# Kernel tuning notes

Hardware: AMD Instinct MI355X
Metric: run time of the kernel (lower is better)

The kernel has to match this reference:

```python
import jax, jax.numpy as jnp
import numpy as np

B, S, H, DH = 2, 2048, 16, 64
D = H * DH


def setup_inputs() -> dict:
    key = jax.random.key(0)
    ks = jax.random.split(key, 10)
    std = 0.02
    return {
        "hidden_states": jax.random.normal(ks[0], (B, S, D), jnp.float32),
        "mask": jax.random.randint(ks[1], (B, S), 0, 2, jnp.int64 if jax.config.jax_enable_x64 else jnp.int32),
        "Wq": jax.random.normal(ks[2], (D, D), jnp.float32) * std,
        "bq": jnp.zeros((D,), jnp.float32),
        "Wk": jax.random.normal(ks[3], (D, D), jnp.float32) * std,
        "bk": jnp.zeros((D,), jnp.float32),
        "Wv": jax.random.normal(ks[4], (D, D), jnp.float32) * std,
        "bv": jnp.zeros((D,), jnp.float32),
        "Wo": jax.random.normal(ks[5], (D, D), jnp.float32) * std,
        "bo": jnp.zeros((D,), jnp.float32),
    }


def _split_heads(x):
    # (B, S, H*DH) -> (B, H, S, DH)
    b, s, _ = x.shape
    return x.reshape(b, s, H, DH).transpose(0, 2, 1, 3)


def reference(hidden_states, mask, Wq, bq, Wk, bk, Wv, bv, Wo, bo):
    # Linear projections (torch nn.Linear: x @ W.T + b)
    q = _split_heads(hidden_states @ Wq.T + bq)
    k = _split_heads(hidden_states @ Wk.T + bk)
    v = _split_heads(hidden_states @ Wv.T + bv)

    scale = 1.0 / np.sqrt(DH).astype(np.float32)
    scores = jnp.einsum("bhqd,bhkd->bhqk", q, k) * scale  # (B,H,S,S)
    # mask out padded key positions (mask==0 -> -inf), broadcast over heads/queries
    scores = jnp.where(mask[:, None, None, :] == 0, -jnp.inf, scores)
    weights = jax.nn.softmax(scores, axis=-1)

    attended = jnp.einsum("bhqk,bhkd->bhqd", weights, v)  # (B,H,S,DH)
    merged = attended.transpose(0, 2, 1, 3).reshape(hidden_states.shape)  # (B,S,D)
    return merged @ Wo.T + bo
```

## Files before the change

### kernel.cpp

```cpp
#include <hip/hip_runtime.h>
#include <hip/hip_bf16.h>

typedef __bf16 bf16;
typedef __bf16 bf16x4 __attribute__((ext_vector_type(4)));
typedef __bf16 bf16x8 __attribute__((ext_vector_type(8)));
typedef float f32x4 __attribute__((ext_vector_type(4)));
typedef unsigned short u16x4 __attribute__((ext_vector_type(4)));

#define B_ 2
#define S_ 2048
#define H_ 16
#define DH_ 64
#define D_ 1024

#define WAIT_VMCNT0() asm volatile("s_waitcnt vmcnt(0)" ::: "memory")
#define WAIT_LGKM0()  asm volatile("s_waitcnt lgkmcnt(0)" ::: "memory")

__device__ __forceinline__ void gld_lds16(const bf16* g, bf16* l) {
    __builtin_amdgcn_global_load_lds(
        (__attribute__((address_space(1))) void*)g,
        (__attribute__((address_space(3))) void*)l, 16, 0, 0);
}

__device__ __forceinline__ bf16 f2bf(float x) {
    union { float f; unsigned u; } v; v.f = x;
    unsigned short h = (unsigned short)((v.u + 0x7FFF + ((v.u >> 16) & 1)) >> 16);
    return __builtin_bit_cast(bf16, h);
}

__device__ __forceinline__ unsigned cvtpk(float lo, float hi) {
    unsigned r;
    asm("v_cvt_pk_bf16_f32 %0, %1, %2" : "=v"(r) : "v"(lo), "v"(hi));
    return r;
}

__device__ __forceinline__ void pl32swap(unsigned &a, unsigned &b) {
    asm("v_permlane32_swap_b32 %0, %1" : "+v"(a), "+v"(b));
}
__device__ __forceinline__ void pl16swap(unsigned &a, unsigned &b) {
    asm("v_permlane16_swap_b32 %0, %1" : "+v"(a), "+v"(b));
}

__global__ __launch_bounds__(256) void cvt_kernel(
    const float* __restrict__ hs,
    const float* __restrict__ Wq, const float* __restrict__ Wk,
    const float* __restrict__ Wv, const float* __restrict__ Wo,
    bf16* __restrict__ hsb, bf16* __restrict__ wqkv, bf16* __restrict__ wob)
{
    int i = (blockIdx.x * 256 + threadIdx.x) * 8;
    const float* src;
    bf16* dst;
    if (i < 4194304) {
        src = hs + i; dst = hsb + i;
    } else if (i < 7340032) {
        int off = i - 4194304;
        int which = off >> 20;
        int within = off & 1048575;
        src = (which == 0 ? Wq : which == 1 ? Wk : Wv) + within;
        dst = wqkv + off;
    } else {
        int off = i - 7340032;
        src = Wo + off; dst = wob + off;
    }
    float4 v0 = *(const float4*)src;
    float4 v1 = *(const float4*)(src + 4);
    bf16x8 o = { (bf16)v0.x, (bf16)v0.y, (bf16)v0.z, (bf16)v0.w,
                 (bf16)v1.x, (bf16)v1.y, (bf16)v1.z, (bf16)v1.w };
    *(bf16x8*)dst = o;
}

__global__ __launch_bounds__(256, 4) void gemm_bt(
    const bf16* __restrict__ A, const bf16* __restrict__ Bm,
    const float* __restrict__ b0, const float* __restrict__ b1,
    const float* __restrict__ b2,
    bf16* __restrict__ Qo, bf16* __restrict__ Ko, bf16* __restrict__ Vt)
{
    const int K = 1024;
    __shared__ __attribute__((aligned(16))) bf16 sA[128 * 64];
    __shared__ __attribute__((aligned(16))) bf16 sB[96 * 64];

    int tid = threadIdx.x;
    int wave = tid >> 6, lane = tid & 63;
    int quad = lane >> 4, l16 = lane & 15;
    int orig = blockIdx.y * 32 + blockIdx.x;
    int xcd = orig & 7, c0 = orig >> 3;
    int mx = (xcd & 3) * 8 + (c0 & 7);
    int ny = (xcd >> 2) * 16 + (c0 >> 3);
    int m0 = mx * 128;
    int n0 = ny * 96;
    int wm = (wave & 1) * 64, wn = (wave >> 1) * 48;
    int fs = l16 & 7;

    f32x4 acc[4][3];
#pragma unroll
    for (int i = 0; i < 4; i++)
#pragma unroll
        for (int j = 0; j < 3; j++) acc[i][j] = (f32x4){0.f, 0.f, 0.f, 0.f};

    for (int k0 = 0; k0 < K; k0 += 64) {
#pragma unroll
        for (int i = 0; i < 4; i++) {
            int c = tid + i * 256;
            int row = c >> 3;
            int kc = ((c & 7) ^ (row & 7)) * 8;
            gld_lds16(A + (size_t)(m0 + row) * K + k0 + kc, &sA[c * 8]);
        }
#pragma unroll
        for (int i = 0; i < 3; i++) {
            int c = tid + i * 256;
            int row = c >> 3;
            int kc = ((c & 7) ^ (row & 7)) * 8;
            gld_lds16(Bm + (size_t)(n0 + row) * K + k0 + kc, &sB[c * 8]);
        }
        WAIT_VMCNT0();
        __syncthreads();

#pragma unroll
        for (int kp = 0; kp < 2; kp++) {
            bf16x8 af[4], bfr[3];
#pragma unroll
            for (int i = 0; i < 4; i++)
                af[i] = *(const bf16x8*)&sA[(wm + i * 16 + l16) * 64 + (((kp * 4 + quad) ^ fs) * 8)];
#pragma unroll
            for (int j = 0; j < 3; j++)
                bfr[j] = *(const bf16x8*)&sB[(wn + j * 16 + l16) * 64 + (((kp * 4 + quad) ^ fs) * 8)];
#pragma unroll
            for (int i = 0; i < 4; i++)
#pragma unroll
                for (int j = 0; j < 3; j++)
                    acc[i][j] = __builtin_amdgcn_mfma_f32_16x16x32_bf16(
                        af[i], bfr[j], acc[i][j], 0, 0, 0);
        }
        __syncthreads();
    }

    const float QSCALE = 0.125f * 1.44269504088896340736f;
#pragma unroll
    for (int j = 0; j < 3; j++) {
        int n = n0 + wn + j * 16 + l16;
        int region = n >> 10;
        int nn = n & 1023;
        int h = nn >> 6, d = nn & 63;
        float bias = (region == 0 ? b0 : region == 1 ? b1 : b2)[nn];
#pragma unroll
        for (int i = 0; i < 4; i++) {
            int mb = m0 + wm + i * 16 + quad * 4;
            int b = mb >> 11, s = mb & 2047;
            int bh = b * H_ + h;
            if (region == 2) {
                bf16x4 pk = { f2bf(acc[i][j][0] + bias), f2bf(acc[i][j][1] + bias),
                              f2bf(acc[i][j][2] + bias), f2bf(acc[i][j][3] + bias) };
                *(bf16x4*)&Vt[((size_t)bh * DH_ + d) * S_ + s] = pk;
            } else {
#pragma unroll
                for (int r = 0; r < 4; r++) {
                    float v = acc[i][j][r] + bias;
                    if (region == 0)
                        Qo[((size_t)bh * S_ + s + r) * DH_ + d] = f2bf(v * QSCALE);
                    else
                        Ko[((size_t)bh * S_ + s + r) * DH_ + d] = f2bf(v);
                }
            }
        }
    }
}

__global__ __launch_bounds__(512, 4) void gemm_out(
    const bf16* __restrict__ A, const bf16* __restrict__ Bm,
    const float* __restrict__ bias0, float* __restrict__ Co)
{
    const int K = 1024;
    __shared__ __attribute__((aligned(16))) bf16 sA[128 * 64];
    __shared__ __attribute__((aligned(16))) bf16 sB[64 * 64];

    int tid = threadIdx.x;
    int wave = tid >> 6, lane = tid & 63;
    int quad = lane >> 4, l16 = lane & 15;
    int orig = blockIdx.y * 32 + blockIdx.x;
    int xcd = orig & 7, c0 = orig >> 3;
    int mx = (xcd & 3) * 8 + (c0 & 7);
    int ny = (xcd >> 2) * 8 + (c0 >> 3);
    int m0 = mx * 128;
    int n0 = ny * 64;
    int wm = (wave & 3) * 32, wn = (wave >> 2) * 32;
    int fs = l16 & 7;

    f32x4 acc[2][2];
#pragma unroll
    for (int i = 0; i < 2; i++)
#pragma unroll
        for (int j = 0; j < 2; j++) acc[i][j] = (f32x4){0.f, 0.f, 0.f, 0.f};

    for (int k0 = 0; k0 < K; k0 += 64) {
#pragma unroll
        for (int i = 0; i < 2; i++) {
            int c = tid + i * 512;
            int row = c >> 3;
            int kc = ((c & 7) ^ (row & 7)) * 8;
            gld_lds16(A + (size_t)(m0 + row) * K + k0 + kc, &sA[c * 8]);
        }
        {
            int c = tid;
            int row = c >> 3;
            int kc = ((c & 7) ^ (row & 7)) * 8;
            gld_lds16(Bm + (size_t)(n0 + row) * K + k0 + kc, &sB[c * 8]);
        }
        WAIT_VMCNT0();
        __syncthreads();

#pragma unroll
        for (int kp = 0; kp < 2; kp++) {
            bf16x8 af[2], bfr[2];
#pragma unroll
            for (int i = 0; i < 2; i++)
                af[i] = *(const bf16x8*)&sA[(wm + i * 16 + l16) * 64 + (((kp * 4 + quad) ^ fs) * 8)];
#pragma unroll
            for (int j = 0; j < 2; j++)
                bfr[j] = *(const bf16x8*)&sB[(wn + j * 16 + l16) * 64 + (((kp * 4 + quad) ^ fs) * 8)];
#pragma unroll
            for (int i = 0; i < 2; i++)
#pragma unroll
                for (int j = 0; j < 2; j++)
                    acc[i][j] = __builtin_amdgcn_mfma_f32_16x16x32_bf16(
                        af[i], bfr[j], acc[i][j], 0, 0, 0);
        }
        __syncthreads();
    }

#pragma unroll
    for (int j = 0; j < 2; j++) {
        int n = n0 + wn + j * 16 + l16;
        float bias = bias0[n];
#pragma unroll
        for (int i = 0; i < 2; i++)
#pragma unroll
            for (int r = 0; r < 4; r++) {
                int m = m0 + wm + i * 16 + quad * 4 + r;
                Co[(size_t)m * D_ + n] = acc[i][j][r] + bias;
            }
    }
}

__global__ __launch_bounds__(256, 4) void attn_kernel(
    const bf16* __restrict__ Q, const bf16* __restrict__ Kg,
    const bf16* __restrict__ Vt, const int* __restrict__ mask,
    bf16* __restrict__ Og)
{
    __shared__ __attribute__((aligned(16))) bf16 sK[128 * 64];
    __shared__ __attribute__((aligned(16))) bf16 sV[64 * 128];
    __shared__ __attribute__((aligned(16))) unsigned short sMadd[S_];

    int tid = threadIdx.x;
    int wave = tid >> 6, lane = tid & 63;
    int quad = lane >> 4, l16 = lane & 15;
    int orig = blockIdx.y * 32 + blockIdx.x;
    int lid = (orig & 7) * 128 + (orig >> 3);
    int bh = lid >> 5;
    int q0 = (lid & 31) * 64;
    int b = bh >> 4;
    int f8 = l16 & 7;
    int qh = wave & 1;
    int kh = wave >> 1;

    const bf16* Qb = Q + (size_t)bh * S_ * DH_;
    const bf16* Kb = Kg + (size_t)bh * S_ * DH_;
    const bf16* Vb = Vt + (size_t)bh * DH_ * S_;

    {
        int base = b * S_ + tid * 8;
        int4 m0 = *(const int4*)&mask[base];
        int4 m1 = *(const int4*)&mask[base + 4];
        u16x4 e0 = { (unsigned short)(m0.x ? 0 : 0xF149),
                     (unsigned short)(m0.y ? 0 : 0xF149),
                     (unsigned short)(m0.z ? 0 : 0xF149),
                     (unsigned short)(m0.w ? 0 : 0xF149) };
        u16x4 e1 = { (unsigned short)(m1.x ? 0 : 0xF149),
                     (unsigned short)(m1.y ? 0 : 0xF149),
                     (unsigned short)(m1.z ? 0 : 0xF149),
                     (unsigned short)(m1.w ? 0 : 0xF149) };
        *(u16x4*)&sMadd[tid * 8] = e0;
        *(u16x4*)&sMadd[tid * 8 + 4] = e1;
    }

    bf16x8 aq[2][2];
#pragma unroll
    for (int qt = 0; qt < 2; qt++) {
        int qrow = q0 + qh * 32 + qt * 16 + l16;
        aq[qt][0] = *(const bf16x8*)&Qb[(size_t)qrow * DH_ + quad * 8];
        aq[qt][1] = *(const bf16x8*)&Qb[(size_t)qrow * DH_ + 32 + quad * 8];
    }

    const bf16 oneb = __builtin_bit_cast(bf16, (unsigned short)0x3F80);
    const bf16x8 ones = { oneb, oneb, oneb, oneb, oneb, oneb, oneb, oneb };

    f32x4 o[2][4];
    f32x4 osum[2];
#pragma unroll
    for (int i = 0; i < 2; i++) {
#pragma unroll
        for (int j = 0; j < 4; j++) o[i][j] = (f32x4){0.f, 0.f, 0.f, 0.f};
        osum[i] = (f32x4){0.f, 0.f, 0.f, 0.f};
    }

    for (int kt = 0; kt < S_; kt += 128) {
#pragma unroll
        for (int i = 0; i < 8; i++) {
            int c = tid + i * 256;
            if (c < 1024) {
                int row = c >> 3;
                int g = (c & 7) ^ (row & 7);
                gld_lds16(&Kb[(size_t)(kt + row) * DH_ + g * 8], &sK[c * 8]);
            } else {
                int cv = c - 1024;
                int row = cv >> 4;
                int g = (cv & 15) ^ (row & 15);
                gld_lds16(&Vb[(size_t)row * S_ + kt + g * 8], &sV[cv * 8]);
            }
        }
        WAIT_VMCNT0();
        __syncthreads();

#pragma unroll
        for (int pass = 0; pass < 2; pass++) {
            unsigned w01[2][2], w23[2][2];
#pragma unroll
            for (int mtl = 0; mtl < 2; mtl++) {
                int keyrow = kh * 64 + pass * 32 + mtl * 16;
                bf16x8 ak0 = *(const bf16x8*)&sK[(keyrow + l16) * 64 + ((quad ^ f8) * 8)];
                bf16x8 ak1 = *(const bf16x8*)&sK[(keyrow + l16) * 64 + (((quad + 4) ^ f8) * 8)];
                u16x4 mm = *(const u16x4*)&sMadd[kt + keyrow + quad * 4];
                f32x4 cinit;
                cinit[0] = __builtin_bit_cast(float, (unsigned)mm.x << 16);
                cinit[1] = __builtin_bit_cast(float, (unsigned)mm.y << 16);
                cinit[2] = __builtin_bit_cast(float, (unsigned)mm.z << 16);
                cinit[3] = __builtin_bit_cast(float, (unsigned)mm.w << 16);
#pragma unroll
                for (int qt = 0; qt < 2; qt++) {
                    f32x4 c = cinit;
                    c = __builtin_amdgcn_mfma_f32_16x16x32_bf16(ak0, aq[qt][0], c, 0, 0, 0);
                    c = __builtin_amdgcn_mfma_f32_16x16x32_bf16(ak1, aq[qt][1], c, 0, 0, 0);
                    float p0 = __builtin_amdgcn_exp2f(c[0]);
                    float p1 = __builtin_amdgcn_exp2f(c[1]);
                    float p2 = __builtin_amdgcn_exp2f(c[2]);
                    float p3 = __builtin_amdgcn_exp2f(c[3]);
                    w01[qt][mtl] = cvtpk(p0, p1);
                    w23[qt][mtl] = cvtpk(p2, p3);
                }
            }

            bf16x8 ap[2];
#pragma unroll
            for (int qt = 0; qt < 2; qt++) {
                unsigned r0 = w01[qt][0], r2 = w01[qt][1];
                pl32swap(r0, r2); pl16swap(r0, r2);
                unsigned r1 = w23[qt][0], r3 = w23[qt][1];
                pl32swap(r1, r3); pl16swap(r1, r3);
                union { unsigned u[4]; bf16x8 v; } U;
                U.u[0] = r0; U.u[1] = r1; U.u[2] = r2; U.u[3] = r3;
                ap[qt] = U.v;
                osum[qt] = __builtin_amdgcn_mfma_f32_16x16x32_bf16(ap[qt], ones, osum[qt], 0, 0, 0);
            }

#pragma unroll
            for (int dt = 0; dt < 4; dt++) {
                int g = (kh * 8 + pass * 4 + quad) ^ l16;
                bf16x8 bv = *(const bf16x8*)&sV[(dt * 16 + l16) * 128 + g * 8];
#pragma unroll
                for (int qt = 0; qt < 2; qt++)
                    o[qt][dt] = __builtin_amdgcn_mfma_f32_16x16x32_bf16(ap[qt], bv, o[qt][dt], 0, 0, 0);
            }
        }
        __syncthreads();
    }

    float* sRed = (wave == 2) ? (float*)sK : (float*)sV;
    if (wave >= 2) {
#pragma unroll
        for (int qt = 0; qt < 2; qt++) {
#pragma unroll
            for (int dt = 0; dt < 4; dt++)
                *(f32x4*)&sRed[((qt * 4 + dt) * 64 + lane) * 4] = o[qt][dt];
            *(f32x4*)&sRed[((8 + qt) * 64 + lane) * 4] = osum[qt];
        }
    }
    __syncthreads();
    if (wave < 2) {
        float* src = (wave == 0) ? (float*)sK : (float*)sV;
#pragma unroll
        for (int qt = 0; qt < 2; qt++) {
#pragma unroll
            for (int dt = 0; dt < 4; dt++)
                o[qt][dt] += *(const f32x4*)&src[((qt * 4 + dt) * 64 + lane) * 4];
            osum[qt] += *(const f32x4*)&src[((8 + qt) * 64 + lane) * 4];
        }
        int h = bh & 15;
#pragma unroll
        for (int qt = 0; qt < 2; qt++) {
            float rcp[4] = { 1.f / osum[qt][0], 1.f / osum[qt][1],
                             1.f / osum[qt][2], 1.f / osum[qt][3] };
#pragma unroll
            for (int r = 0; r < 4; r++) {
                int s = q0 + wave * 32 + qt * 16 + quad * 4 + r;
#pragma unroll
                for (int dt = 0; dt < 4; dt++) {
                    int d = dt * 16 + l16;
                    Og[((size_t)(b * S_ + s)) * D_ + h * 64 + d] = f2bf(o[qt][dt][r] * rcp[r]);
                }
            }
        }
    }
}

extern "C" void kernel_launch(void* const* d_in, const int* in_sizes, int n_in,
                              void* d_out, int out_size, void* d_ws, size_t ws_size,
                              hipStream_t stream) {
    const float* hs = (const float*)d_in[0];
    const int* mask = (const int*)d_in[1];
    const float* Wq = (const float*)d_in[2];
    const float* bq = (const float*)d_in[3];
    const float* Wk = (const float*)d_in[4];
    const float* bk = (const float*)d_in[5];
    const float* Wv = (const float*)d_in[6];
    const float* bv = (const float*)d_in[7];
    const float* Wo = (const float*)d_in[8];
    const float* bo = (const float*)d_in[9];
    float* out = (float*)d_out;

    char* ws = (char*)d_ws;
    bf16* hsb  = (bf16*)(ws);
    bf16* wqkv = (bf16*)(ws + ((size_t)8 << 20));
    bf16* wob  = (bf16*)(ws + ((size_t)14 << 20));
    bf16* Qw   = (bf16*)(ws + ((size_t)16 << 20));
    bf16* Kw   = (bf16*)(ws + ((size_t)24 << 20));
    bf16* Vtw  = (bf16*)(ws + ((size_t)32 << 20));
    bf16* attn = (bf16*)(ws + ((size_t)40 << 20));

    cvt_kernel<<<4096, 256, 0, stream>>>(hs, Wq, Wk, Wv, Wo, hsb, wqkv, wob);
    gemm_bt<<<dim3(32, 32), 256, 0, stream>>>(hsb, wqkv, bq, bk, bv,
                                              Qw, Kw, Vtw);
    attn_kernel<<<dim3(32, 32), 256, 0, stream>>>(Qw, Kw, Vtw, mask, attn);
    gemm_out<<<dim3(32, 16), 512, 0, stream>>>(attn, wob, bo, out);
}
```

Baseline: 186.5 us.

## Switch projection GEMMs to 32x32x16 MFMA and retile QKV GEMM to 128x64

Both projection GEMMs move from 16x16x32 bf16 MFMA to the larger 32x32x16 bf16 MFMA, with new LDS fragment indexing and epilogue output mapping. The QKV GEMM tile shrinks from 128x96 to 128x64 with a 32x48 grid and occupancy hint raised to 6 blocks. The aim is fewer LDS reads per MFMA and more resident blocks. Smaller N tiles in the QKV GEMM mean more A-tile reloads and lower arithmetic intensity per block.

Result: no change. 186.5 us (-0.0%).

```diff
diff --git a/kernel.cpp b/kernel.cpp
--- a/kernel.cpp
+++ b/kernel.cpp
@@ -5,6 +5,7 @@
 typedef __bf16 bf16x4 __attribute__((ext_vector_type(4)));
 typedef __bf16 bf16x8 __attribute__((ext_vector_type(8)));
 typedef float f32x4 __attribute__((ext_vector_type(4)));
+typedef float f32x16 __attribute__((ext_vector_type(16)));
 typedef unsigned short u16x4 __attribute__((ext_vector_type(4)));
 
 #define B_ 2
@@ -69,7 +70,7 @@
     *(bf16x8*)dst = o;
 }
 
-__global__ __launch_bounds__(256, 4) void gemm_bt(
+__global__ __launch_bounds__(256, 6) void gemm_bt(
     const bf16* __restrict__ A, const bf16* __restrict__ Bm,
     const float* __restrict__ b0, const float* __restrict__ b1,
     const float* __restrict__ b2,
@@ -77,25 +78,25 @@
 {
     const int K = 1024;
     __shared__ __attribute__((aligned(16))) bf16 sA[128 * 64];
-    __shared__ __attribute__((aligned(16))) bf16 sB[96 * 64];
+    __shared__ __attribute__((aligned(16))) bf16 sB[64 * 64];
 
     int tid = threadIdx.x;
     int wave = tid >> 6, lane = tid & 63;
-    int quad = lane >> 4, l16 = lane & 15;
+    int l32 = lane & 31, hl = lane >> 5;
+    int f8b = l32 & 7;
     int orig = blockIdx.y * 32 + blockIdx.x;
     int xcd = orig & 7, c0 = orig >> 3;
     int mx = (xcd & 3) * 8 + (c0 & 7);
-    int ny = (xcd >> 2) * 16 + (c0 >> 3);
+    int ny = (xcd >> 2) * 24 + (c0 >> 3);
     int m0 = mx * 128;
-    int n0 = ny * 96;
-    int wm = (wave & 1) * 64, wn = (wave >> 1) * 48;
-    int fs = l16 & 7;
-
-    f32x4 acc[4][3];
-#pragma unroll
-    for (int i = 0; i < 4; i++)
-#pragma unroll
-        for (int j = 0; j < 3; j++) acc[i][j] = (f32x4){0.f, 0.f, 0.f, 0.f};
+    int n0 = ny * 64;
+    int wm = (wave & 1) * 64, wn = (wave >> 1) * 32;
+
+    f32x16 acc[2];
+#pragma unroll
+    for (int i = 0; i < 2; i++)
+#pragma unroll
+        for (int r = 0; r < 16; r++) acc[i][r] = 0.f;
 
     for (int k0 = 0; k0 < K; k0 += 64) {
 #pragma unroll
@@ -106,7 +107,7 @@
             gld_lds16(A + (size_t)(m0 + row) * K + k0 + kc, &sA[c * 8]);
         }
 #pragma unroll
-        for (int i = 0; i < 3; i++) {
+        for (int i = 0; i < 2; i++) {
             int c = tid + i * 256;
             int row = c >> 3;
             int kc = ((c & 7) ^ (row & 7)) * 8;
@@ -116,45 +117,38 @@
         __syncthreads();
 
 #pragma unroll
-        for (int kp = 0; kp < 2; kp++) {
-            bf16x8 af[4], bfr[3];
-#pragma unroll
-            for (int i = 0; i < 4; i++)
-                af[i] = *(const bf16x8*)&sA[(wm + i * 16 + l16) * 64 + (((kp * 4 + quad) ^ fs) * 8)];
-#pragma unroll
-            for (int j = 0; j < 3; j++)
-                bfr[j] = *(const bf16x8*)&sB[(wn + j * 16 + l16) * 64 + (((kp * 4 + quad) ^ fs) * 8)];
-#pragma unroll
-            for (int i = 0; i < 4; i++)
-#pragma unroll
-                for (int j = 0; j < 3; j++)
-                    acc[i][j] = __builtin_amdgcn_mfma_f32_16x16x32_bf16(
-                        af[i], bfr[j], acc[i][j], 0, 0, 0);
+        for (int kk = 0; kk < 4; kk++) {
+            int gsel = ((kk * 2 + hl) ^ f8b) * 8;
+            bf16x8 bf = *(const bf16x8*)&sB[(wn + l32) * 64 + gsel];
+            bf16x8 af0 = *(const bf16x8*)&sA[(wm + l32) * 64 + gsel];
+            bf16x8 af1 = *(const bf16x8*)&sA[(wm + 32 + l32) * 64 + gsel];
+            acc[0] = __builtin_amdgcn_mfma_f32_32x32x16_bf16(af0, bf, acc[0], 0, 0, 0);
+            acc[1] = __builtin_amdgcn_mfma_f32_32x32x16_bf16(af1, bf, acc[1], 0, 0, 0);
         }
         __syncthreads();
     }
 
     const float QSCALE = 0.125f * 1.44269504088896340736f;
-#pragma unroll
-    for (int j = 0; j < 3; j++) {
-        int n = n0 + wn + j * 16 + l16;
-        int region = n >> 10;
-        int nn = n & 1023;
-        int h = nn >> 6, d = nn & 63;
-        float bias = (region == 0 ? b0 : region == 1 ? b1 : b2)[nn];
-#pragma unroll
-        for (int i = 0; i < 4; i++) {
-            int mb = m0 + wm + i * 16 + quad * 4;
+    int n = n0 + wn + l32;
+    int region = n >> 10;
+    int nn = n & 1023;
+    int h = nn >> 6, d = nn & 63;
+    float bias = (region == 0 ? b0 : region == 1 ? b1 : b2)[nn];
+#pragma unroll
+    for (int i = 0; i < 2; i++) {
+#pragma unroll
+        for (int g = 0; g < 4; g++) {
+            int mb = m0 + wm + i * 32 + g * 8 + hl * 4;
             int b = mb >> 11, s = mb & 2047;
             int bh = b * H_ + h;
             if (region == 2) {
-                bf16x4 pk = { f2bf(acc[i][j][0] + bias), f2bf(acc[i][j][1] + bias),
-                              f2bf(acc[i][j][2] + bias), f2bf(acc[i][j][3] + bias) };
+                bf16x4 pk = { f2bf(acc[i][4 * g + 0] + bias), f2bf(acc[i][4 * g + 1] + bias),
+                              f2bf(acc[i][4 * g + 2] + bias), f2bf(acc[i][4 * g + 3] + bias) };
                 *(bf16x4*)&Vt[((size_t)bh * DH_ + d) * S_ + s] = pk;
             } else {
 #pragma unroll
                 for (int r = 0; r < 4; r++) {
-                    float v = acc[i][j][r] + bias;
+                    float v = acc[i][4 * g + r] + bias;
                     if (region == 0)
                         Qo[((size_t)bh * S_ + s + r) * DH_ + d] = f2bf(v * QSCALE);
                     else
@@ -175,7 +169,8 @@
 
     int tid = threadIdx.x;
     int wave = tid >> 6, lane = tid & 63;
-    int quad = lane >> 4, l16 = lane & 15;
+    int l32 = lane & 31, hl = lane >> 5;
+    int f8b = l32 & 7;
     int orig = blockIdx.y * 32 + blockIdx.x;
     int xcd = orig & 7, c0 = orig >> 3;
     int mx = (xcd & 3) * 8 + (c0 & 7);
@@ -183,13 +178,10 @@
     int m0 = mx * 128;
     int n0 = ny * 64;
     int wm = (wave & 3) * 32, wn = (wave >> 2) * 32;
-    int fs = l16 & 7;
-
-    f32x4 acc[2][2];
-#pragma unroll
-    for (int i = 0; i < 2; i++)
-#pragma unroll
-        for (int j = 0; j < 2; j++) acc[i][j] = (f32x4){0.f, 0.f, 0.f, 0.f};
+
+    f32x16 acc;
+#pragma unroll
+    for (int r = 0; r < 16; r++) acc[r] = 0.f;
 
     for (int k0 = 0; k0 < K; k0 += 64) {
 #pragma unroll
@@ -209,35 +201,23 @@
         __syncthreads();
 
 #pragma unroll
-        for (int kp = 0; kp < 2; kp++) {
-            bf16x8 af[2], bfr[2];
-#pragma unroll
-            for (int i = 0; i < 2; i++)
-                af[i] = *(const bf16x8*)&sA[(wm + i * 16 + l16) * 64 + (((kp * 4 + quad) ^ fs) * 8)];
-#pragma unroll
-            for (int j = 0; j < 2; j++)
-                bfr[j] = *(const bf16x8*)&sB[(wn + j * 16 + l16) * 64 + (((kp * 4 + quad) ^ fs) * 8)];
-#pragma unroll
-            for (int i = 0; i < 2; i++)
-#pragma unroll
-                for (int j = 0; j < 2; j++)
-                    acc[i][j] = __builtin_amdgcn_mfma_f32_16x16x32_bf16(
-                        af[i], bfr[j], acc[i][j], 0, 0, 0);
-        }
-        __syncthreads();
-    }
-
-#pragma unroll
-    for (int j = 0; j < 2; j++) {
-        int n = n0 + wn + j * 16 + l16;
-        float bias = bias0[n];
-#pragma unroll
-        for (int i = 0; i < 2; i++)
-#pragma unroll
-            for (int r = 0; r < 4; r++) {
-                int m = m0 + wm + i * 16 + quad * 4 + r;
-                Co[(size_t)m * D_ + n] = acc[i][j][r] + bias;
-            }
+        for (int kk = 0; kk < 4; kk++) {
+            int gsel = ((kk * 2 + hl) ^ f8b) * 8;
+            bf16x8 af = *(const bf16x8*)&sA[(wm + l32) * 64 + gsel];
+            bf16x8 bf = *(const bf16x8*)&sB[(wn + l32) * 64 + gsel];
+            acc = __builtin_amdgcn_mfma_f32_32x32x16_bf16(af, bf, acc, 0, 0, 0);
+        }
+        __syncthreads();
+    }
+
+    int n = n0 + wn + l32;
+    float bias = bias0[n];
+#pragma unroll
+    for (int g = 0; g < 4; g++) {
+        int m = m0 + wm + g * 8 + hl * 4;
+#pragma unroll
+        for (int r = 0; r < 4; r++)
+            Co[(size_t)(m + r) * D_ + n] = acc[4 * g + r] + bias;
     }
 }
 
@@ -436,7 +416,7 @@
     bf16* attn = (bf16*)(ws + ((size_t)40 << 20));
 
     cvt_kernel<<<4096, 256, 0, stream>>>(hs, Wq, Wk, Wv, Wo, hsb, wqkv, wob);
-    gemm_bt<<<dim3(32, 32), 256, 0, stream>>>(hsb, wqkv, bq, bk, bv,
+    gemm_bt<<<dim3(32, 48), 256, 0, stream>>>(hsb, wqkv, bq, bk, bv,
                                               Qw, Kw, Vtw);
     attn_kernel<<<dim3(32, 32), 256, 0, stream>>>(Qw, Kw, Vtw, mask, attn);
     gemm_out<<<dim3(32, 16), 512, 0, stream>>>(attn, wob, bo, out);
```
